# Kernel optimization log

Hardware: AMD Instinct MI355X
Metric: run time of the kernel (lower is better)

Reference implementation:

```python
import jax, jax.numpy as jnp
import numpy as np

HID = 512
ALPHA = 0.01
PI = np.float32(np.pi)


def _mlp(x, W0, b0, W1, b1, W2, b2, W3, b3):
    # x: [..., 2] -> scalar field u(x): [...]
    h = jnp.tanh(x @ W0 + b0)
    h = jnp.tanh(h @ W1 + b1)
    h = jnp.tanh(h @ W2 + b2)
    return (h @ W3 + b3)[..., 0]


def _forcing(x):
    # f = -Delta u for u = sin(pi x) sin(pi y^2)
    xx, yy = x[:, 0], x[:, 1]
    return (-PI ** 2 * (1 + 4 * yy ** 2) * jnp.sin(PI * xx) * jnp.sin(PI * yy ** 2)
            + 2 * PI * jnp.sin(PI * xx) * jnp.cos(PI * yy ** 2))


def setup_inputs() -> dict:
    key = jax.random.key(0)
    ks = jax.random.split(key, 6)
    n_i, n_b = 20000, 800
    x_interior = jax.random.uniform(ks[0], (n_i, 2), dtype=jnp.float32)  # domain (0,1)
    theta = jnp.linspace(0.0, 2.0 * np.pi, n_b)
    x_boundary = jnp.stack([(jnp.cos(theta) + 1.0) * 0.5,
                            (jnp.sin(theta) + 1.0) * 0.5], axis=1).astype(jnp.float32)

    def w(k, shape, fan_in):
        return (jax.random.normal(k, shape, jnp.float32) / np.float32(np.sqrt(fan_in)))

    W0 = w(ks[1], (2, HID), 2)
    b0 = jnp.zeros((HID,), jnp.float32)
    W1 = w(ks[2], (HID, HID), HID)
    b1 = jnp.zeros((HID,), jnp.float32)
    W2 = w(ks[3], (HID, HID), HID)
    b2 = jnp.zeros((HID,), jnp.float32)
    W3 = w(ks[4], (HID, 1), HID)
    b3 = jnp.zeros((1,), jnp.float32)
    return dict(x_interior=x_interior, x_boundary=x_boundary,
                W0=W0, b0=b0, W1=W1, b1=b1, W2=W2, b2=b2, W3=W3, b3=b3)


def reference(x_interior, x_boundary, W0, b0, W1, b1, W2, b2, W3, b3):
    params = (W0, b0, W1, b1, W2, b2, W3, b3)

    def u_scalar(x):  # x: [2] -> scalar
        return _mlp(x, *params)

    g = jax.grad(u_scalar)

    def lap_one(x):
        # Laplacian = trace of Hessian via forward-over-reverse HVPs
        lap = jnp.float32(0.0)
        for i in range(2):
            e = jnp.zeros((2,), x.dtype).at[i].set(1.0)
            _, hv = jax.jvp(g, (x,), (e,))
            lap = lap + hv[i]
        return lap

    laplacian = jax.vmap(lap_one)(x_interior)  # [n_interior]
    interior_loss = jnp.mean((laplacian - _forcing(x_interior)) ** 2)
    boundary_loss = jnp.mean(_mlp(x_boundary, *params) ** 2)
    total_loss = ALPHA * interior_loss + boundary_loss
    return total_loss, interior_loss, boundary_loss
```

## Files before the change

kernel.cpp:

```cpp
#include <hip/hip_runtime.h>
#include <math.h>

#define HID 512
#define KP 520
#define PPB 32

typedef __attribute__((ext_vector_type(8))) _Float16 half8;
typedef __attribute__((ext_vector_type(4))) _Float16 half4;
typedef __attribute__((ext_vector_type(4))) float f32x4;

static __device__ __forceinline__ float fast_tanh(float x) {
    float e = __expf(2.f * x);
    return 1.f - 2.f / (e + 1.f);
}

__global__ __launch_bounds__(256) void prep_wt(
    const float* __restrict__ W, _Float16* __restrict__ Wh)
{
    int gid = blockIdx.x * 256 + threadIdx.x;
    int k8   = gid & 7;
    int quad = (gid >> 3) & 3;
    int l15  = (gid >> 5) & 15;
    int kb   = (gid >> 9) & 15;
    int jb   = gid >> 13;
    int j = jb * 16 + l15;
    int k = kb * 32 + quad * 8 + k8;
    Wh[gid] = (_Float16)W[k * HID + j];
}

template<bool FULL>
static __device__ __forceinline__ void layer_pass(
    const _Float16* __restrict__ Wh, const float* __restrict__ bias,
    _Float16 (*Als)[PPB][KP], int wv, int lane)
{
    const int l15 = lane & 15, quad = lane >> 4;
    const int j0w = wv * 64;
    const int jb0 = wv * 4;
    const int foff = l15 * 32 + quad * 8;

    f32x4 acc[4][2][4];
    #pragma unroll
    for (int s = 0; s < 4; ++s)
        #pragma unroll
        for (int pf = 0; pf < 2; ++pf)
            #pragma unroll
            for (int jt = 0; jt < 4; ++jt) acc[s][pf][jt] = (f32x4)0.f;

    half8 wA[4], wB[4];
    #pragma unroll
    for (int jt = 0; jt < 4; ++jt)
        wA[jt] = *(const half8*)(Wh + (size_t)((jb0 + jt) * 16) * 512 + foff);

    auto iter = [&](int kb, half8 (&wc)[4], half8 (&wn)[4]) {
        half8 a[2][4];
        #pragma unroll
        for (int pf = 0; pf < 2; ++pf)
            #pragma unroll
            for (int s = 0; s < 4; ++s)
                a[pf][s] = *(const half8*)&Als[s][pf * 16 + l15][kb * 32 + quad * 8];
        if (kb < 15) {
            #pragma unroll
            for (int jt = 0; jt < 4; ++jt)
                wn[jt] = *(const half8*)(Wh + (size_t)((jb0 + jt) * 16 + kb + 1) * 512 + foff);
        }
        #pragma unroll
        for (int s = 0; s < 4; ++s)
            #pragma unroll
            for (int pf = 0; pf < 2; ++pf)
                #pragma unroll
                for (int jt = 0; jt < 4; ++jt)
                    acc[s][pf][jt] = __builtin_amdgcn_mfma_f32_16x16x32_f16(
                        wc[jt], a[pf][s], acc[s][pf][jt], 0, 0, 0);
    };

    #pragma unroll
    for (int kb = 0; kb < 16; kb += 2) {
        iter(kb,     wA, wB);
        iter(kb + 1, wB, wA);
    }

    __syncthreads();

    #pragma unroll
    for (int jt = 0; jt < 4; ++jt) {
        const int jbase = j0w + jt * 16 + quad * 4;
        f32x4 bv = *(const f32x4*)&bias[jbase];
        #pragma unroll
        for (int pf = 0; pf < 2; ++pf) {
            const int p = pf * 16 + l15;
            half4 vh, vt1, vt2, vS;
            #pragma unroll
            for (int r = 0; r < 4; ++r) {
                float a  = fast_tanh(acc[0][pf][jt][r] + bv[r]);
                float g  = 1.f - a * a;
                float z1 = acc[1][pf][jt][r];
                float z2 = acc[2][pf][jt][r];
                vh[r] = (_Float16)a;
                if (FULL) {
                    vt1[r] = (_Float16)(g * z1);
                    vt2[r] = (_Float16)(g * z2);
                }
                vS[r] = (_Float16)(g * acc[3][pf][jt][r] - 2.f * a * g * (z1 * z1 + z2 * z2));
            }
            *(half4*)&Als[0][p][jbase] = vh;
            if (FULL) {
                *(half4*)&Als[1][p][jbase] = vt1;
                *(half4*)&Als[2][p][jbase] = vt2;
            }
            *(half4*)&Als[3][p][jbase] = vS;
        }
    }
    __syncthreads();
}

__global__ __launch_bounds__(512) void pois_fused(
    const float* __restrict__ x_int, const float* __restrict__ x_bnd,
    const float* __restrict__ W0, const float* __restrict__ b0,
    const _Float16* __restrict__ W1h, const float* __restrict__ b1,
    const _Float16* __restrict__ W2h, const float* __restrict__ b2,
    const float* __restrict__ W3, const float* __restrict__ b3,
    float* __restrict__ partials, int NI, int NT, int nblk)
{
    __shared__ _Float16 Als[4][PPB][KP];
    __shared__ float sc[64];

    const int tid = threadIdx.x;
    const int wv = tid >> 6, lane = tid & 63;
    const int p0 = blockIdx.x * PPB;

    {
        const int p = tid & 31, kc = tid >> 5;
        int gp = p0 + p;
        int gpc = (gp >= NT) ? 0 : gp;
        float xx, yy;
        if (gpc < NI) { xx = x_int[2 * gpc];        yy = x_int[2 * gpc + 1]; }
        else          { xx = x_bnd[2 * (gpc - NI)]; yy = x_bnd[2 * (gpc - NI) + 1]; }
        #pragma unroll
        for (int k8 = 0; k8 < 4; ++k8) {
            const int k = kc * 32 + k8 * 8;
            f32x4 w0a = *(const f32x4*)&W0[k],       w0b = *(const f32x4*)&W0[k + 4];
            f32x4 w1a = *(const f32x4*)&W0[HID + k], w1b = *(const f32x4*)&W0[HID + k + 4];
            f32x4 b0a = *(const f32x4*)&b0[k],       b0b = *(const f32x4*)&b0[k + 4];
            half8 vh, vt1, vt2, vS;
            #pragma unroll
            for (int i = 0; i < 8; ++i) {
                float w0i = (i < 4) ? w0a[i] : w0b[i - 4];
                float w1i = (i < 4) ? w1a[i] : w1b[i - 4];
                float bbi = (i < 4) ? b0a[i] : b0b[i - 4];
                float a = fast_tanh(xx * w0i + yy * w1i + bbi);
                float g = 1.f - a * a;
                vh[i]  = (_Float16)a;
                vt1[i] = (_Float16)(g * w0i);
                vt2[i] = (_Float16)(g * w1i);
                vS[i]  = (_Float16)(-2.f * a * g * (w0i * w0i + w1i * w1i));
            }
            *(half8*)&Als[0][p][k] = vh;
            *(half8*)&Als[1][p][k] = vt1;
            *(half8*)&Als[2][p][k] = vt2;
            *(half8*)&Als[3][p][k] = vS;
        }
    }
    __syncthreads();

    layer_pass<true >(W1h, b1, Als, wv, lane);
    layer_pass<false>(W2h, b2, Als, wv, lane);

    {
        const int psub = lane >> 4, kc = lane & 15;
        const int p = wv * 4 + psub;
        float u = 0.f, lap = 0.f;
        #pragma unroll
        for (int k8 = 0; k8 < 4; ++k8) {
            const int k = kc * 32 + k8 * 8;
            half8 hh = *(const half8*)&Als[0][p][k];
            half8 ss = *(const half8*)&Als[3][p][k];
            f32x4 wa = *(const f32x4*)&W3[k], wb = *(const f32x4*)&W3[k + 4];
            #pragma unroll
            for (int i = 0; i < 8; ++i) {
                float w = (i < 4) ? wa[i] : wb[i - 4];
                u   += (float)hh[i] * w;
                lap += (float)ss[i] * w;
            }
        }
        #pragma unroll
        for (int off = 1; off < 16; off <<= 1) {
            u   += __shfl_xor(u, off);
            lap += __shfl_xor(lap, off);
        }
        if (kc == 0) {
            int gp = p0 + p;
            float vi = 0.f, vb = 0.f;
            if (gp < NI) {
                const float PIf = 3.14159265358979323846f;
                float xx = x_int[2 * gp], yy = x_int[2 * gp + 1];
                float sx = sinf(PIf * xx);
                float y2 = yy * yy;
                float sy = sinf(PIf * y2), cy = cosf(PIf * y2);
                float f = -PIf * PIf * (1.f + 4.f * y2) * sx * sy + 2.f * PIf * sx * cy;
                float r = lap - f;
                vi = r * r;
            } else if (gp < NT) {
                float uu = u + b3[0];
                vb = uu * uu;
            }
            sc[p * 2] = vi; sc[p * 2 + 1] = vb;
        }
    }
    __syncthreads();
    if (tid == 0) {
        float svi = 0.f, svb = 0.f;
        #pragma unroll
        for (int p = 0; p < PPB; ++p) { svi += sc[p * 2]; svb += sc[p * 2 + 1]; }
        partials[blockIdx.x] = svi;
        partials[nblk + blockIdx.x] = svb;
    }
}

__global__ __launch_bounds__(256) void pois_reduce(
    const float* __restrict__ partials, float* __restrict__ out,
    int nblk, int NI, int NB)
{
    int tid = threadIdx.x;
    float si = 0.f, sb = 0.f;
    for (int i = tid; i < nblk; i += 256) {
        si += partials[i];
        sb += partials[nblk + i];
    }
    #pragma unroll
    for (int off = 32; off > 0; off >>= 1) {
        si += __shfl_xor(si, off);
        sb += __shfl_xor(sb, off);
    }
    __shared__ float ri[4], rb[4];
    int wv = tid >> 6;
    if ((tid & 63) == 0) { ri[wv] = si; rb[wv] = sb; }
    __syncthreads();
    if (tid == 0) {
        float inter = (ri[0] + ri[1] + ri[2] + ri[3]) / (float)NI;
        float bound = (rb[0] + rb[1] + rb[2] + rb[3]) / (float)NB;
        out[0] = 0.01f * inter + bound;
        out[1] = inter;
        out[2] = bound;
    }
}

extern "C" void kernel_launch(void* const* d_in, const int* in_sizes, int n_in,
                              void* d_out, int out_size, void* d_ws, size_t ws_size,
                              hipStream_t stream)
{
    const float* x_int = (const float*)d_in[0];
    const float* x_bnd = (const float*)d_in[1];
    const float* W0 = (const float*)d_in[2];
    const float* b0 = (const float*)d_in[3];
    const float* W1 = (const float*)d_in[4];
    const float* b1 = (const float*)d_in[5];
    const float* W2 = (const float*)d_in[6];
    const float* b2 = (const float*)d_in[7];
    const float* W3 = (const float*)d_in[8];
    const float* b3 = (const float*)d_in[9];

    int NI = in_sizes[0] / 2;
    int NB = in_sizes[1] / 2;
    int NT = NI + NB;
    int nblk = (NT + PPB - 1) / PPB;

    float* partials = (float*)d_ws;
    _Float16* W1h = (_Float16*)((char*)d_ws + 16384);
    _Float16* W2h = W1h + 262144;

    prep_wt<<<1024, 256, 0, stream>>>(W1, W1h);
    prep_wt<<<1024, 256, 0, stream>>>(W2, W2h);

    pois_fused<<<nblk, 512, 0, stream>>>(
        x_int, x_bnd, W0, b0, W1h, b1, W2h, b2, W3, b3,
        partials, NI, NT, nblk);

    pois_reduce<<<1, 256, 0, stream>>>(partials, (float*)d_out, nblk, NI, NB);
}
```

Baseline: 180.8 us.

## Halve points per block, widen per-wave output tile, merge weight prep launches

Changes the fused kernel to 16 points per block with 256 threads (4 waves), each wave now computing 128 output columns with 8 MFMA column tiles instead of 64 columns over two 16-point halves. This doubles the block count for better CU fill (about 1300 blocks versus about 650) and allows two blocks per CU via launch bounds. The cost is that each weight fragment loaded from global/L2 is reused across only 16 points instead of 32, which doubles total weight traffic. The two weight-conversion launches are also merged into one launch. The remaining lines of the kernel (layer 0 init, output reduction) are partly hidden and must match the new thread count.

```diff
diff --git a/kernel.cpp b/kernel.cpp
--- a/kernel.cpp
+++ b/kernel.cpp
@@ -3,7 +3,7 @@
 
 #define HID 512
 #define KP 520
-#define PPB 32
+#define PPB 16
 
 typedef __attribute__((ext_vector_type(8))) _Float16 half8;
 typedef __attribute__((ext_vector_type(4))) _Float16 half4;
@@ -15,9 +15,13 @@
 }
 
 __global__ __launch_bounds__(256) void prep_wt(
-    const float* __restrict__ W, _Float16* __restrict__ Wh)
-{
-    int gid = blockIdx.x * 256 + threadIdx.x;
+    const float* __restrict__ W1, const float* __restrict__ W2,
+    _Float16* __restrict__ W1h, _Float16* __restrict__ W2h)
+{
+    int b = blockIdx.x;
+    const float* W = (b < 1024) ? W1 : W2;
+    _Float16* Wh   = (b < 1024) ? W1h : W2h;
+    int gid = (b & 1023) * 256 + threadIdx.x;
     int k8   = gid & 7;
     int quad = (gid >> 3) & 3;
     int l15  = (gid >> 5) & 15;
@@ -34,43 +38,37 @@
     _Float16 (*Als)[PPB][KP], int wv, int lane)
 {
     const int l15 = lane & 15, quad = lane >> 4;
-    const int j0w = wv * 64;
-    const int jb0 = wv * 4;
+    const int j0w = wv * 128;
+    const int jb0 = wv * 8;
     const int foff = l15 * 32 + quad * 8;
 
-    f32x4 acc[4][2][4];
+    f32x4 acc[4][8];
     #pragma unroll
     for (int s = 0; s < 4; ++s)
         #pragma unroll
-        for (int pf = 0; pf < 2; ++pf)
-            #pragma unroll
-            for (int jt = 0; jt < 4; ++jt) acc[s][pf][jt] = (f32x4)0.f;
-
-    half8 wA[4], wB[4];
-    #pragma unroll
-    for (int jt = 0; jt < 4; ++jt)
+        for (int jt = 0; jt < 8; ++jt) acc[s][jt] = (f32x4)0.f;
+
+    half8 wA[8], wB[8];
+    #pragma unroll
+    for (int jt = 0; jt < 8; ++jt)
         wA[jt] = *(const half8*)(Wh + (size_t)((jb0 + jt) * 16) * 512 + foff);
 
-    auto iter = [&](int kb, half8 (&wc)[4], half8 (&wn)[4]) {
-        half8 a[2][4];
-        #pragma unroll
-        for (int pf = 0; pf < 2; ++pf)
-            #pragma unroll
-            for (int s = 0; s < 4; ++s)
-                a[pf][s] = *(const half8*)&Als[s][pf * 16 + l15][kb * 32 + quad * 8];
+    auto iter = [&](int kb, half8 (&wc)[8], half8 (&wn)[8]) {
+        half8 a[4];
+        #pragma unroll
+        for (int s = 0; s < 4; ++s)
+            a[s] = *(const half8*)&Als[s][l15][kb * 32 + quad * 8];
         if (kb < 15) {
             #pragma unroll
-            for (int jt = 0; jt < 4; ++jt)
+            for (int jt = 0; jt < 8; ++jt)
                 wn[jt] = *(const half8*)(Wh + (size_t)((jb0 + jt) * 16 + kb + 1) * 512 + foff);
         }
         #pragma unroll
         for (int s = 0; s < 4; ++s)
             #pragma unroll
-            for (int pf = 0; pf < 2; ++pf)
-                #pragma unroll
-                for (int jt = 0; jt < 4; ++jt)
-                    acc[s][pf][jt] = __builtin_amdgcn_mfma_f32_16x16x32_f16(
-                        wc[jt], a[pf][s], acc[s][pf][jt], 0, 0, 0);
+            for (int jt = 0; jt < 8; ++jt)
+                acc[s][jt] = __builtin_amdgcn_mfma_f32_16x16x32_f16(
+                    wc[jt], a[s], acc[s][jt], 0, 0, 0);
     };
 
     #pragma unroll
@@ -82,38 +80,34 @@
     __syncthreads();
 
     #pragma unroll
-    for (int jt = 0; jt < 4; ++jt) {
+    for (int jt = 0; jt < 8; ++jt) {
         const int jbase = j0w + jt * 16 + quad * 4;
         f32x4 bv = *(const f32x4*)&bias[jbase];
-        #pragma unroll
-        for (int pf = 0; pf < 2; ++pf) {
-            const int p = pf * 16 + l15;
-            half4 vh, vt1, vt2, vS;
-            #pragma unroll
-            for (int r = 0; r < 4; ++r) {
-                float a  = fast_tanh(acc[0][pf][jt][r] + bv[r]);
-                float g  = 1.f - a * a;
-                float z1 = acc[1][pf][jt][r];
-                float z2 = acc[2][pf][jt][r];
-                vh[r] = (_Float16)a;
-                if (FULL) {
-                    vt1[r] = (_Float16)(g * z1);
-                    vt2[r] = (_Float16)(g * z2);
-                }
-                vS[r] = (_Float16)(g * acc[3][pf][jt][r] - 2.f * a * g * (z1 * z1 + z2 * z2));
-            }
-            *(half4*)&Als[0][p][jbase] = vh;
+        half4 vh, vt1, vt2, vS;
+        #pragma unroll
+        for (int r = 0; r < 4; ++r) {
+            float a  = fast_tanh(acc[0][jt][r] + bv[r]);
+            float g  = 1.f - a * a;
+            float z1 = acc[1][jt][r];
+            float z2 = acc[2][jt][r];
+            vh[r] = (_Float16)a;
             if (FULL) {
-                *(half4*)&Als[1][p][jbase] = vt1;
-                *(half4*)&Als[2][p][jbase] = vt2;
-            }
-            *(half4*)&Als[3][p][jbase] = vS;
-        }
-    }
-    __syncthreads();
-}
-
-__global__ __launch_bounds__(512) void pois_fused(
+                vt1[r] = (_Float16)(g * z1);
+                vt2[r] = (_Float16)(g * z2);
+            }
+            vS[r] = (_Float16)(g * acc[3][jt][r] - 2.f * a * g * (z1 * z1 + z2 * z2));
+        }
+        *(half4*)&Als[0][l15][jbase] = vh;
+        if (FULL) {
+            *(half4*)&Als[1][l15][jbase] = vt1;
+            *(half4*)&Als[2][l15][jbase] = vt2;
+        }
+        *(half4*)&Als[3][l15][jbase] = vS;
+    }
+    __syncthreads();
+}
+
+__global__ __launch_bounds__(256, 2) void pois_fused(
     const float* __restrict__ x_int, const float* __restrict__ x_bnd,
     const float* __restrict__ W0, const float* __restrict__ b0,
     const _Float16* __restrict__ W1h, const float* __restrict__ b1,
@@ -122,14 +116,14 @@
     float* __restrict__ partials, int NI, int NT, int nblk)
 {
     __shared__ _Float16 Als[4][PPB][KP];
-    __shared__ float sc[64];
+    __shared__ float sc[32];
 
     const int tid = threadIdx.x;
     const int wv = tid >> 6, lane = tid & 63;
     const int p0 = blockIdx.x * PPB;
 
     {
-        const int p = tid & 31, kc = tid >> 5;
+        const int p = tid & 15, kc = tid >> 4;
         int gp = p0 + p;
         int gpc = (gp >= NT) ? 0 : gp;
         float xx, yy;
@@ -268,10 +262,9 @@
     _Float16* W1h = (_Float16*)((char*)d_ws + 16384);
     _Float16* W2h = W1h + 262144;
 
-    prep_wt<<<1024, 256, 0, stream>>>(W1, W1h);
-    prep_wt<<<1024, 256, 0, stream>>>(W2, W2h);
-
-    pois_fused<<<nblk, 512, 0, stream>>>(
+    prep_wt<<<2048, 256, 0, stream>>>(W1, W2, W1h, W2h);
+
+    pois_fused<<<nblk, 256, 0, stream>>>(
         x_int, x_bnd, W0, b0, W1h, b1, W2h, b2, W3, b3,
         partials, NI, NT, nblk);
 
```

Measured after the change: 205.9 us. +13.9%, slower.
